# Optimization experiments

Measured on AMD Instinct MI355X. Metric: run time of the kernel, lower is better.

Reference implementation:

```python
import jax, jax.numpy as jnp
import numpy as np

B, N, S, D, H, ITERS = 32, 4096, 24, 256, 4, 3
DH = D // H
SCALE = DH ** -0.5
EPS = 1e-8
LN_EPS = 1e-5


def _ln(x, g, b):
    m = x.mean(-1, keepdims=True)
    v = ((x - m) ** 2).mean(-1, keepdims=True)
    return (x - m) * jax.lax.rsqrt(v + LN_EPS) * g + b


def setup_inputs() -> dict:
    key = jax.random.key(0)
    ks = jax.random.split(key, 20)
    xav = lambda k, fi, fo: jax.random.uniform(k, (fi, fo), jnp.float32, -1.0, 1.0) * np.sqrt(6.0 / (fi + fo))
    u = lambda k, shp, fan: jax.random.uniform(k, shp, jnp.float32, -1.0, 1.0) / np.sqrt(fan)
    return {
        "extracted_features": jax.random.normal(ks[0], (B, N, D), jnp.float32),
        "conditioning": jax.random.normal(ks[1], (B, S, D), jnp.float32),
        "pos_ln_g": jnp.ones((D,), jnp.float32),
        "pos_ln_b": jnp.zeros((D,), jnp.float32),
        "pos_w1": xav(ks[2], D, D),
        "pos_b1": jnp.zeros((D,), jnp.float32),
        "pos_w2": xav(ks[3], D, D),
        "pos_b2": jnp.zeros((D,), jnp.float32),
        "in_ln_g": jnp.ones((D,), jnp.float32),
        "in_ln_b": jnp.zeros((D,), jnp.float32),
        "slot_ln_g": jnp.ones((D,), jnp.float32),
        "slot_ln_b": jnp.zeros((D,), jnp.float32),
        "Wq": u(ks[4], (D, D), D),
        "Wk": u(ks[5], (D, D), D),
        "Wv": u(ks[6], (D, D), D),
        "gru_wi": u(ks[7], (D, 3 * D), D),  # x @ gru_wi, torch weight_ih.T
        "gru_wh": u(ks[8], (D, 3 * D), D),
        "gru_bi": u(ks[9], (3 * D,), D),
        "gru_bh": u(ks[10], (3 * D,), D),
    }


def reference(extracted_features, conditioning, pos_ln_g, pos_ln_b, pos_w1, pos_b1,
              pos_w2, pos_b2, in_ln_g, in_ln_b, slot_ln_g, slot_ln_b,
              Wq, Wk, Wv, gru_wi, gru_wh, gru_bi, gru_bh):
    b, n, _ = extracted_features.shape
    s = conditioning.shape[1]
    # positional embedding MLP: LN -> Linear -> ReLU -> Linear
    feats = _ln(extracted_features, pos_ln_g, pos_ln_b)
    feats = jax.nn.relu(feats @ pos_w1 + pos_b1) @ pos_w2 + pos_b2
    # slot attention input norm + k/v projections
    inp = _ln(feats, in_ln_g, in_ln_b)
    k = (inp @ Wk).reshape(b, n, H, DH)
    v = (inp @ Wv).reshape(b, n, H, DH)

    slots = conditioning
    attn_before = None
    for _ in range(ITERS):
        slots_prev = slots
        sn = _ln(slots, slot_ln_g, slot_ln_b)
        q = (sn @ Wq).reshape(b, s, H, DH)
        dots = jnp.einsum('bihd,bjhd->bihj', q, k) * SCALE  # [b,s,H,n]
        # softmax over flattened (slot, head) axis per input token
        attn = jax.nn.softmax(dots.reshape(b, s * H, n), axis=1).reshape(b, s, H, n)
        attn_before = attn
        attn_r = (attn + EPS)
        attn_r = attn_r / attn_r.sum(-1, keepdims=True)
        updates = jnp.einsum('bjhd,bihj->bihd', v, attn_r).reshape(b * s, D)
        # GRUCell update
        h = slots_prev.reshape(b * s, D)
        gi = updates @ gru_wi + gru_bi
        gh = h @ gru_wh + gru_bh
        ir, iz, inn = jnp.split(gi, 3, axis=-1)
        hr, hz, hn = jnp.split(gh, 3, axis=-1)
        r = jax.nn.sigmoid(ir + hr)
        z = jax.nn.sigmoid(iz + hz)
        nn_ = jnp.tanh(inn + r * hn)
        slots = ((1.0 - z) * nn_ + z * h).reshape(b, s, D)

    return slots, attn_before.mean(axis=2)
```

## Files before the change

### kernel.cpp

```cpp
#include <hip/hip_runtime.h>
#include <hip/hip_bf16.h>
#include <stdint.h>

typedef __hip_bfloat16 bf16;
typedef __attribute__((ext_vector_type(8))) short short8;
typedef __attribute__((ext_vector_type(4))) float floatx4;

#define DEV __device__ __forceinline__

DEV float bf2f(bf16 v) { return __bfloat162float(v); }
DEV bf16 f2b(float f) { return __float2bfloat16(f); }
DEV unsigned short f2bu(float f) {
  bf16 h = __float2bfloat16(f);
  union { bf16 h; unsigned short u; } c; c.h = h; return c.u;
}
DEV bool is_bf16_in(const void* probe) { return ((const unsigned short*)probe)[0] != 0; }


__global__ __launch_bounds__(256) void params_kernel(
    const void* s0, const void* s1, const void* s2, const void* s3, const void* s4,
    const void* s5, const void* s6, const void* s7, const void* s8, const void* s9,
    float* dst)
{
  int idx = blockIdx.x * 256 + threadIdx.x;
  if (idx >= 3584) return;
  bool bf = is_bf16_in(s0);
  const void* srcs[10] = {s0, s1, s2, s3, s4, s5, s6, s7, s8, s9};
  int a, off;
  if (idx < 2048)      { a = idx >> 8; off = idx & 255; }
  else if (idx < 2816) { a = 8; off = idx - 2048; }
  else                 { a = 9; off = idx - 2816; }
  float v = bf ? bf2f(((const bf16*)srcs[a])[off]) : ((const float*)srcs[a])[off];
  dst[idx] = v;
}

__global__ __launch_bounds__(256) void transpose_all_kernel(
    const void* w1, const void* w2, const void* wq, const void* wk, const void* wv,
    const void* gwi, const void* gwh,
    bf16* d1, bf16* d2, bf16* dq, bf16* dk, bf16* dv, bf16* dgi, bf16* dgh,
    const void* probe)
{
  int idx = blockIdx.x * 256 + threadIdx.x;
  if (idx >= 720896) return;
  bool bf = is_bf16_in(probe);
  const void* src; bf16* dst; int C, off;
  if (idx < 327680) {
    int wsel = idx >> 16; off = idx & 65535; C = 256;
    const void* S[5] = {w1, w2, wq, wk, wv};
    bf16* D[5] = {d1, d2, dq, dk, dv};
    src = S[wsel]; dst = D[wsel];
  } else {
    int j = idx - 327680; int wsel = j / 196608; off = j - wsel * 196608; C = 768;
    src = wsel ? gwh : gwi; dst = wsel ? dgh : dgi;
  }
  int r = off / C, c = off - r * C;
  bf16 v = bf ? ((const bf16*)src)[off] : f2b(((const float*)src)[off]);
  dst[(size_t)c * 256 + r] = v;
}

__global__ __launch_bounds__(256) void init_slots_kernel(
    const void* __restrict__ cond, float* __restrict__ sF, bf16* __restrict__ sB,
    const void* probe)
{
  int idx = blockIdx.x * 256 + threadIdx.x;
  bool bf = is_bf16_in(probe);
  float v = bf ? bf2f(((const bf16*)cond)[idx]) : ((const float*)cond)[idx];
  sF[idx] = v;
  sB[idx] = f2b(v);
}

template<bool OUT_BF16, bool RELU, bool HAS_BIAS>
DEV void gemm_body(const bf16* __restrict__ A, const bf16* __restrict__ Bt,
                   const float* __restrict__ bias, void* __restrict__ C,
                   int M, int N, int K, int bx, int by, short* As, short* Bs)
{
  const int tid = threadIdx.x;
  const int lane = tid & 63;
  const int wave = tid >> 6;
  const int wr = wave >> 1, wc = wave & 1;
  const int m16 = lane & 15, quad = lane >> 4;
  const long m0 = (long)by * 128, n0 = (long)bx * 128;

  floatx4 acc[4][4];
#pragma unroll
  for (int i = 0; i < 4; i++)
#pragma unroll
    for (int j = 0; j < 4; j++) acc[i][j] = {0.f, 0.f, 0.f, 0.f};

  const int srow = tid >> 3;
  const int scol = (tid & 7) * 8;

  for (int kb = 0; kb < K; kb += 64) {
#pragma unroll
    for (int p = 0; p < 4; p++) {
      int row = srow + p * 32;
      uint4 av = *(const uint4*)(A + (m0 + row) * (long)K + kb + scol);
      *(uint4*)(&As[row * 72 + scol]) = av;
      uint4 bv = *(const uint4*)(Bt + (n0 + row) * (long)K + kb + scol);
      *(uint4*)(&Bs[row * 72 + scol]) = bv;
    }
    __syncthreads();
#pragma unroll
    for (int ks = 0; ks < 2; ks++) {
      short8 af[4], bfr[4];
#pragma unroll
      for (int t = 0; t < 4; t++) {
        af[t]  = *(const short8*)(&As[(wr * 64 + t * 16 + m16) * 72 + ks * 32 + quad * 8]);
        bfr[t] = *(const short8*)(&Bs[(wc * 64 + t * 16 + m16) * 72 + ks * 32 + quad * 8]);
      }
#pragma unroll
      for (int mt = 0; mt < 4; mt++)
#pragma unroll
        for (int nt = 0; nt < 4; nt++)
          acc[mt][nt] = __builtin_amdgcn_mfma_f32_16x16x32_bf16(af[mt], bfr[nt], acc[mt][nt], 0, 0, 0);
    }
    __syncthreads();
  }

#pragma unroll
  for (int mt = 0; mt < 4; mt++) {
#pragma unroll
    for (int nt = 0; nt < 4; nt++) {
      long col = n0 + wc * 64 + nt * 16 + m16;
      float bb = HAS_BIAS ? bias[col] : 0.f;
#pragma unroll
      for (int r = 0; r < 4; r++) {
        long row = m0 + wr * 64 + mt * 16 + quad * 4 + r;
        float v = acc[mt][nt][r] + bb;
        if (RELU) v = fmaxf(v, 0.f);
        if (OUT_BF16) ((bf16*)C)[row * N + col] = f2b(v);
        else          ((float*)C)[row * N + col] = v;
      }
    }
  }
}

__global__ __launch_bounds__(256) void gru2_kernel(
    const bf16* __restrict__ updB, const bf16* __restrict__ sB,
    const bf16* __restrict__ gwit, const bf16* __restrict__ gwht,
    const float* __restrict__ par, float* __restrict__ gi, float* __restrict__ gh)
{
  __shared__ short As[128 * 72];
  __shared__ short Bs[128 * 72];
  if (blockIdx.z == 0)
    gemm_body<false, false, true>(updB, gwit, par + 2048, gi, 768, 768, 256,
                                  blockIdx.x, blockIdx.y, As, Bs);
  else
    gemm_body<false, false, true>(sB, gwht, par + 2816, gh, 768, 768, 256,
                                  blockIdx.x, blockIdx.y, As, Bs);
}


DEV void mm64(const short* As, const bf16* __restrict__ W,
              floatx4 acc[4][4], int wave, int m16, int quad)
{
#pragma unroll
  for (int ks = 0; ks < 8; ks++) {
    short8 af[4], bfr[4];
#pragma unroll
    for (int t = 0; t < 4; t++) {
      int row = t * 16 + m16;
      af[t] = *(const short8*)(&As[row * 256 + ((ks * 32 + quad * 8) ^ ((row & 7) << 3))]);
      bfr[t] = *(const short8*)(W + (size_t)(wave * 64 + t * 16 + m16) * 256 + ks * 32 + quad * 8);
    }
#pragma unroll
    for (int mt = 0; mt < 4; mt++)
#pragma unroll
      for (int nt = 0; nt < 4; nt++)
        acc[mt][nt] = __builtin_amdgcn_mfma_f32_16x16x32_bf16(af[mt], bfr[nt], acc[mt][nt], 0, 0, 0);
  }
}

__global__ __launch_bounds__(256, 3) void phasea_kernel(
    const void* __restrict__ x,
    const bf16* __restrict__ w1t, const bf16* __restrict__ w2t,
    const bf16* __restrict__ wkt, const bf16* __restrict__ wvt,
    const float* __restrict__ par,
    bf16* __restrict__ kbuf, bf16* __restrict__ vT, const void* probe)
{
  __shared__ short As[64 * 256];
  const int tid = threadIdx.x;
  const int lane = tid & 63;
  const int wave = tid >> 6;
  const int m16 = lane & 15, quad = lane >> 4;
  const long m0 = (long)blockIdx.x * 64;
  const bool bfin = is_bf16_in(probe);

  {
    float4 gv = *(const float4*)(par + lane * 4);
    float4 bv = *(const float4*)(par + 256 + lane * 4);
#pragma unroll
    for (int i = 0; i < 16; i++) {
      int row = wave * 16 + i;
      float v[4];
      if (bfin) {
        uint2 u = *(const uint2*)((const bf16*)x + (m0 + row) * 256 + lane * 4);
        v[0] = __uint_as_float((u.x & 0xffffu) << 16);
        v[1] = __uint_as_float(u.x & 0xffff0000u);
        v[2] = __uint_as_float((u.y & 0xffffu) << 16);
        v[3] = __uint_as_float(u.y & 0xffff0000u);
      } else {
        float4 f = *(const float4*)((const float*)x + (m0 + row) * 256 + lane * 4);
        v[0] = f.x; v[1] = f.y; v[2] = f.z; v[3] = f.w;
      }
      float s = v[0] + v[1] + v[2] + v[3];
      float sq = v[0] * v[0] + v[1] * v[1] + v[2] * v[2] + v[3] * v[3];
#pragma unroll
      for (int off = 32; off > 0; off >>= 1) { s += __shfl_xor(s, off); sq += __shfl_xor(sq, off); }
      float mn = s * (1.f / 256.f);
      float rs = rsqrtf(sq * (1.f / 256.f) - mn * mn + 1e-5f);
      union { unsigned short us[4]; uint2 u; } pk;
      pk.us[0] = f2bu((v[0] - mn) * rs * gv.x + bv.x);
      pk.us[1] = f2bu((v[1] - mn) * rs * gv.y + bv.y);
      pk.us[2] = f2bu((v[2] - mn) * rs * gv.z + bv.z);
      pk.us[3] = f2bu((v[3] - mn) * rs * gv.w + bv.w);
      *(uint2*)(&As[row * 256 + ((lane * 4) ^ ((row & 7) << 3))]) = pk.u;
    }
  }
  __syncthreads();

  floatx4 acc[4][4];

#pragma unroll
  for (int i = 0; i < 4; i++)
#pragma unroll
    for (int j = 0; j < 4; j++) acc[i][j] = {0.f, 0.f, 0.f, 0.f};
  mm64(As, w1t, acc, wave, m16, quad);
  __syncthreads();
#pragma unroll
  for (int mt = 0; mt < 4; mt++)
#pragma unroll
    for (int nt = 0; nt < 4; nt++) {
      int col = wave * 64 + nt * 16 + m16;
      float bb = par[512 + col];
#pragma unroll
      for (int r = 0; r < 4; r++) {
        int row = mt * 16 + quad * 4 + r;
        As[row * 256 + (col ^ ((row & 7) << 3))] = (short)f2bu(fmaxf(acc[mt][nt][r] + bb, 0.f));
      }
    }
  __syncthreads();

#pragma unroll
  for (int i = 0; i < 4; i++)
#pragma unroll
    for (int j = 0; j < 4; j++) acc[i][j] = {0.f, 0.f, 0.f, 0.f};
  mm64(As, w2t, acc, wave, m16, quad);
  __syncthreads();
#pragma unroll
  for (int mt = 0; mt < 4; mt++)
#pragma unroll
    for (int nt = 0; nt < 4; nt++) {
      int col = wave * 64 + nt * 16 + m16;
      float bb = par[768 + col];
#pragma unroll
      for (int r = 0; r < 4; r++) {
        int row = mt * 16 + quad * 4 + r;
        As[row * 256 + (col ^ ((row & 7) << 3))] = (short)f2bu(acc[mt][nt][r] + bb);
      }
    }
  __syncthreads();

  {
    float4 gv = *(const float4*)(par + 1024 + lane * 4);
    float4 bv = *(const float4*)(par + 1280 + lane * 4);
#pragma unroll
    for (int i = 0; i < 16; i++) {
      int row = wave * 16 + i;
      int ci = (lane * 4) ^ ((row & 7) << 3);
      uint2 u = *(const uint2*)(&As[row * 256 + ci]);
      float v[4];
      v[0] = __uint_as_float((u.x & 0xffffu) << 16);
      v[1] = __uint_as_float(u.x & 0xffff0000u);
      v[2] = __uint_as_float((u.y & 0xffffu) << 16);
      v[3] = __uint_as_float(u.y & 0xffff0000u);
      float s = v[0] + v[1] + v[2] + v[3];
      float sq = v[0] * v[0] + v[1] * v[1] + v[2] * v[2] + v[3] * v[3];
#pragma unroll
      for (int off = 32; off > 0; off >>= 1) { s += __shfl_xor(s, off); sq += __shfl_xor(sq, off); }
      float mn = s * (1.f / 256.f);
      float rs = rsqrtf(sq * (1.f / 256.f) - mn * mn + 1e-5f);
      union { unsigned short us[4]; uint2 u; } pk;
      pk.us[0] = f2bu((v[0] - mn) * rs * gv.x + bv.x);
      pk.us[1] = f2bu((v[1] - mn) * rs * gv.y + bv.y);
      pk.us[2] = f2bu((v[2] - mn) * rs * gv.z + bv.z);
      pk.us[3] = f2bu((v[3] - mn) * rs * gv.w + bv.w);
      *(uint2*)(&As[row * 256 + ci]) = pk.u;
    }
  }
  __syncthreads();

#pragma unroll
  for (int i = 0; i < 4; i++)
#pragma unroll
    for (int j = 0; j < 4; j++) acc[i][j] = {0.f, 0.f, 0.f, 0.f};
  mm64(As, wkt, acc, wave, m16, quad);
#pragma unroll
  for (int mt = 0; mt < 4; mt++)
#pragma unroll
    for (int nt = 0; nt < 4; nt++) {
      int col = wave * 64 + nt * 16 + m16;
#pragma unroll
      for (int r = 0; r < 4; r++) {
        long row = m0 + mt * 16 + quad * 4 + r;
        kbuf[row * 256 + col] = f2b(acc[mt][nt][r]);
      }
    }

#pragma unroll
  for (int i = 0; i < 4; i++)
#pragma unroll
    for (int j = 0; j < 4; j++) acc[i][j] = {0.f, 0.f, 0.f, 0.f};
  mm64(As, wvt, acc, wave, m16, quad);
  __syncthreads();
#pragma unroll
  for (int mt = 0; mt < 4; mt++)
#pragma unroll
    for (int nt = 0; nt < 4; nt++) {
      int d = wave * 64 + nt * 16 + m16;
      int t = mt * 16 + quad * 4;
      union { unsigned short us[4]; uint2 u; } pk;
#pragma unroll
      for (int r = 0; r < 4; r++) pk.us[r] = f2bu(acc[mt][nt][r]);
      *(uint2*)(&As[d * 64 + (t ^ ((d & 15) << 2))]) = pk.u;
    }
  __syncthreads();

  {
    int sub = lane >> 4;
    int mcol = lane & 15;
#pragma unroll
    for (int j = 0; j < 16; j++) {
      int d = wave * 64 + j * 4 + sub;
      int t = mcol * 4;
      uint2 u = *(const uint2*)(&As[d * 64 + (t ^ ((d & 15) << 2))]);
      *(uint2*)(vT + (size_t)d * 131072 + m0 + t) = u;
    }
  }
}

__global__ __launch_bounds__(256) void lnq_kernel(
    const float* __restrict__ sF, const bf16* __restrict__ wqt,
    const float* __restrict__ par, bf16* __restrict__ qp)
{
  __shared__ short As[32 * 264];
  const int tid = threadIdx.x;
  const int lane = tid & 63;
  const int wave = tid >> 6;
  const int m16 = lane & 15, quad = lane >> 4;
  const int b = blockIdx.x;

  for (int i = tid; i < 8 * 264; i += 256) As[24 * 264 + i] = 0;

  float4 gv = *(const float4*)(par + 1536 + lane * 4);
  float4 bv = *(const float4*)(par + 1792 + lane * 4);
#pragma unroll
  for (int i = 0; i < 6; i++) {
    int row = wave * 6 + i;
    float4 f = *(const float4*)(sF + ((size_t)(b * 24 + row)) * 256 + lane * 4);
    float v[4] = {f.x, f.y, f.z, f.w};
    float s = v[0] + v[1] + v[2] + v[3];
    float sq = v[0] * v[0] + v[1] * v[1] + v[2] * v[2] + v[3] * v[3];
#pragma unroll
    for (int off = 32; off > 0; off >>= 1) { s += __shfl_xor(s, off); sq += __shfl_xor(sq, off); }
    float mn = s * (1.f / 256.f);
    float rs = rsqrtf(sq * (1.f / 256.f) - mn * mn + 1e-5f);
    union { unsigned short us[4]; uint2 u; } pk;
    pk.us[0] = f2bu((v[0] - mn) * rs * gv.x + bv.x);
    pk.us[1] = f2bu((v[1] - mn) * rs * gv.y + bv.y);
    pk.us[2] = f2bu((v[2] - mn) * rs * gv.z + bv.z);
    pk.us[3] = f2bu((v[3] - mn) * rs * gv.w + bv.w);
    *(uint2*)(&As[row * 264 + lane * 4]) = pk.u;
  }
  __syncthreads();

  floatx4 acc[2][4];
#pragma unroll
  for (int i = 0; i < 2; i++)
#pragma unroll
    for (int j = 0; j < 4; j++) acc[i][j] = {0.f, 0.f, 0.f, 0.f};
#pragma unroll
  for (int ks = 0; ks < 8; ks++) {
    short8 af[2], bfr[4];
#pragma unroll
    for (int mt = 0; mt < 2; mt++)
      af[mt] = *(const short8*)(&As[(mt * 16 + m16) * 264 + ks * 32 + quad * 8]);
#pragma unroll
    for (int nt = 0; nt < 4; nt++)
      bfr[nt] = *(const short8*)(wqt + (size_t)(wave * 64 + nt * 16 + m16) * 256 + ks * 32 + quad * 8);
#pragma unroll
    for (int mt = 0; mt < 2; mt++)
#pragma unroll
      for (int nt = 0; nt < 4; nt++)
        acc[mt][nt] = __builtin_amdgcn_mfma_f32_16x16x32_bf16(af[mt], bfr[nt], acc[mt][nt], 0, 0, 0);
  }

  bf16* qpb = qp + (size_t)(b * 4 + wave) * 2048;
#pragma unroll
  for (int mt = 0; mt < 2; mt++)
#pragma unroll
    for (int nt = 0; nt < 4; nt++)
#pragma unroll
      for (int r = 0; r < 4; r++) {
        int m = mt * 16 + quad * 4 + r;
        qpb[m * 64 + nt * 16 + m16] = f2b(acc[mt][nt][r] * 0.125f);
      }
}

template<bool LAST>
__global__ __launch_bounds__(256) void attn_iter_kernel(
    const bf16* __restrict__ qp, const bf16* __restrict__ kbuf,
    const bf16* __restrict__ vT, float* __restrict__ pupd,
    void* __restrict__ out, const void* __restrict__ probe)
{
  const int js = blockIdx.x;
  const int b  = blockIdx.y;
  const int h  = threadIdx.x >> 6;
  const int lane = threadIdx.x & 63;
  const int m16 = lane & 15, quad = lane >> 4;

  __shared__ unsigned short att[4 * 24 * 136];
  __shared__ float red1[4 * 132];
  __shared__ float red2[4 * 132];

  short8 qf[2][2];
  const bf16* qpb = qp + (size_t)(b * 4 + h) * 2048;
#pragma unroll
  for (int mt = 0; mt < 2; mt++)
#pragma unroll
    for (int ks = 0; ks < 2; ks++)
      qf[mt][ks] = *(const short8*)(qpb + (mt * 16 + m16) * 64 + ks * 32 + quad * 8);

  const bool mt1_valid = (quad < 2);
  int arow1 = 16 + m16; if (arow1 > 23) arow1 = 23;

  floatx4 uacc[2][4];
#pragma unroll
  for (int i = 0; i < 2; i++)
#pragma unroll
    for (int j = 0; j < 4; j++) uacc[i][j] = {0.f, 0.f, 0.f, 0.f};
  float wsum[2][4] = {{0.f, 0.f, 0.f, 0.f}, {0.f, 0.f, 0.f, 0.f}};

  for (int hh = 0; hh < 2; hh++) {
    const int j0 = js * 256 + hh * 128;

    floatx4 dacc[2][8];
#pragma unroll
    for (int i = 0; i < 2; i++)
#pragma unroll
      for (int j = 0; j < 8; j++) dacc[i][j] = {0.f, 0.f, 0.f, 0.f};

    const bf16* kb = kbuf + ((size_t)b * 4096 + j0) * 256 + h * 64;
#pragma unroll
    for (int ks = 0; ks < 2; ks++)
#pragma unroll
      for (int nt = 0; nt < 8; nt++) {
        short8 bfr = *(const short8*)(kb + (size_t)(nt * 16 + m16) * 256 + ks * 32 + quad * 8);
        dacc[0][nt] = __builtin_amdgcn_mfma_f32_16x16x32_bf16(qf[0][ks], bfr, dacc[0][nt], 0, 0, 0);
        dacc[1][nt] = __builtin_amdgcn_mfma_f32_16x16x32_bf16(qf[1][ks], bfr, dacc[1][nt], 0, 0, 0);
      }

    float cmax[8];
#pragma unroll
    for (int nt = 0; nt < 8; nt++) {
      float m = fmaxf(fmaxf(dacc[0][nt][0], dacc[0][nt][1]), fmaxf(dacc[0][nt][2], dacc[0][nt][3]));
      if (mt1_valid)
        m = fmaxf(m, fmaxf(fmaxf(dacc[1][nt][0], dacc[1][nt][1]), fmaxf(dacc[1][nt][2], dacc[1][nt][3])));
      m = fmaxf(m, __shfl_xor(m, 16));
      m = fmaxf(m, __shfl_xor(m, 32));
      cmax[nt] = m;
    }
    if (quad == 0) {
#pragma unroll
      for (int nt = 0; nt < 8; nt++) red1[h * 132 + nt * 16 + m16] = cmax[nt];
    }
    __syncthreads();

    float csum[8];
#pragma unroll
    for (int nt = 0; nt < 8; nt++) {
      int c = nt * 16 + m16;
      float g = fmaxf(fmaxf(red1[c], red1[132 + c]), fmaxf(red1[264 + c], red1[396 + c]));
      float s = 0.f;
#pragma unroll
      for (int r = 0; r < 4; r++) {
        float e = __expf(dacc[0][nt][r] - g);
        dacc[0][nt][r] = e; s += e;
      }
#pragma unroll
      for (int r = 0; r < 4; r++) {
        float e = mt1_valid ? __expf(dacc[1][nt][r] - g) : 0.f;
        dacc[1][nt][r] = e; s += e;
      }
      s += __shfl_xor(s, 16);
      s += __shfl_xor(s, 32);
      csum[nt] = s;
    }
    if (quad == 0) {
#pragma unroll
      for (int nt = 0; nt < 8; nt++) red2[h * 132 + nt * 16 + m16] = csum[nt];
    }
    __syncthreads();

#pragma unroll
    for (int nt = 0; nt < 8; nt++) {
      int c = nt * 16 + m16;
      float inv = 1.f / (red2[c] + red2[132 + c] + red2[264 + c] + red2[396 + c]);
#pragma unroll
      for (int r = 0; r < 4; r++) {
        float a = dacc[0][nt][r] * inv + 1e-8f;
        att[h * 3264 + (quad * 4 + r) * 136 + c] = f2bu(a);
        wsum[0][r] += a;
      }
      if (mt1_valid) {
#pragma unroll
        for (int r = 0; r < 4; r++) {
          float a = dacc[1][nt][r] * inv + 1e-8f;
          att[h * 3264 + (16 + quad * 4 + r) * 136 + c] = f2bu(a);
          wsum[1][r] += a;
        }
      }
    }
    __syncthreads();

    const bf16* vb0 = vT + (size_t)b * 4096 + j0;
#pragma unroll
    for (int ks = 0; ks < 4; ks++) {
      short8 a0 = *(const short8*)(&att[h * 3264 + m16 * 136 + ks * 32 + quad * 8]);
      short8 a1 = *(const short8*)(&att[h * 3264 + arow1 * 136 + ks * 32 + quad * 8]);
#pragma unroll
      for (int nt = 0; nt < 4; nt++) {
        short8 bfr = *(const short8*)(vb0 + (size_t)(h * 64 + nt * 16 + m16) * 131072 + ks * 32 + quad * 8);
        uacc[0][nt] = __builtin_amdgcn_mfma_f32_16x16x32_bf16(a0, bfr, uacc[0][nt], 0, 0, 0);
        uacc[1][nt] = __builtin_amdgcn_mfma_f32_16x16x32_bf16(a1, bfr, uacc[1][nt], 0, 0, 0);
      }
    }

    if (LAST) {
      const bool bfo = is_bf16_in(probe);
      int c = threadIdx.x & 127;
      int half = threadIdx.x >> 7;
#pragma unroll
      for (int i0 = 0; i0 < 12; i0++) {
        int i = half * 12 + i0;
        float s = bf2f(__ushort_as_bfloat16(att[i * 136 + c]))
                + bf2f(__ushort_as_bfloat16(att[3264 + i * 136 + c]))
                + bf2f(__ushort_as_bfloat16(att[6528 + i * 136 + c]))
                + bf2f(__ushort_as_bfloat16(att[9792 + i * 136 + c]));
        size_t oidx = ((size_t)(b * 24 + i)) * 4096 + j0 + c;
        if (bfo) ((bf16*)out)[196608 + oidx] = f2b(0.25f * s);
        else     ((float*)out)[196608 + oidx] = 0.25f * s;
      }
    }
    __syncthreads();
  }

  float* dst = pupd + ((size_t)((b * 4 + h) * 16 + js)) * 1920;
#pragma unroll
  for (int mt = 0; mt < 2; mt++)
#pragma unroll
    for (int r = 0; r < 4; r++) {
      float w = wsum[mt][r];
      w += __shfl_xor(w, 1); w += __shfl_xor(w, 2);
      w += __shfl_xor(w, 4); w += __shfl_xor(w, 8);
      wsum[mt][r] = w;
    }
  if (m16 == 0) {
#pragma unroll
    for (int mt = 0; mt < 2; mt++)
#pragma unroll
      for (int r = 0; r < 4; r++) {
        int row = mt * 16 + quad * 4 + r;
        if (row < 24) dst[row * 80 + 64] = wsum[mt][r];
      }
  }
#pragma unroll
  for (int mt = 0; mt < 2; mt++)
#pragma unroll
    for (int nt = 0; nt < 4; nt++)
#pragma unroll
      for (int r = 0; r < 4; r++) {
        int row = mt * 16 + quad * 4 + r;
        if (row < 24) dst[row * 80 + nt * 16 + m16] = uacc[mt][nt][r];
      }
}

__global__ __launch_bounds__(256) void upd_final_kernel(
    const float* __restrict__ pupd, bf16* __restrict__ updB)
{
  int bh = blockIdx.x; int b = bh >> 2, h = bh & 3;
  int idx = blockIdx.y * 256 + threadIdx.x;
  int i = idx >> 6, d = idx & 63;
  const float* base = pupd + (size_t)bh * 16 * 1920 + i * 80;
  float v = 0.f, w = 0.f;
#pragma unroll
  for (int p = 0; p < 16; p++) {
    v += base[p * 1920 + d];
    w += base[p * 1920 + 64];
  }
  updB[((size_t)(b * 24 + i)) * 256 + h * 64 + d] = f2b(v / w);
}

template<bool LAST>
__global__ __launch_bounds__(256) void gru_gate_kernel(
    const float* __restrict__ gi, const float* __restrict__ gh,
    float* __restrict__ sF, bf16* __restrict__ sB,
    void* __restrict__ out, const void* __restrict__ probe)
{
  int row = blockIdx.x, d = threadIdx.x;
  size_t o = (size_t)row * 768;
  float ir = gi[o + d], iz = gi[o + 256 + d], inn = gi[o + 512 + d];
  float hr = gh[o + d], hz = gh[o + 256 + d], hn = gh[o + 512 + d];
  float hv = sF[(size_t)row * 256 + d];
  float r = 1.f / (1.f + __expf(-(ir + hr)));
  float z = 1.f / (1.f + __expf(-(iz + hz)));
  float nn = tanhf(inn + r * hn);
  float sv = (1.f - z) * nn + z * hv;
  sF[(size_t)row * 256 + d] = sv;
  sB[(size_t)row * 256 + d] = f2b(sv);
  if (LAST) {
    if (is_bf16_in(probe)) ((bf16*)out)[(size_t)row * 256 + d] = f2b(sv);
    else                   ((float*)out)[(size_t)row * 256 + d] = sv;
  }
}

static constexpr size_t SZ_BIG   = (size_t)32 * 4096 * 256 * 2;
static constexpr size_t OFF_BUF1 = 0;
static constexpr size_t OFF_BUF2 = OFF_BUF1 + SZ_BIG;
static constexpr size_t OFF_K    = OFF_BUF2 + SZ_BIG;
static constexpr size_t OFF_V    = OFF_K + SZ_BIG;
static constexpr size_t OFF_Q    = OFF_V + SZ_BIG;
static constexpr size_t OFF_QP   = OFF_Q + (size_t)768 * 256 * 4;
static constexpr size_t OFF_SNB  = OFF_QP + (size_t)32 * 4 * 32 * 64 * 2;
static constexpr size_t OFF_SF   = OFF_SNB + (size_t)768 * 256 * 2;
static constexpr size_t OFF_SB   = OFF_SF + (size_t)768 * 256 * 4;
static constexpr size_t OFF_UPD  = OFF_SB + (size_t)768 * 256 * 2;
static constexpr size_t OFF_GI   = OFF_UPD + (size_t)768 * 256 * 2;
static constexpr size_t OFF_GH   = OFF_GI + (size_t)768 * 768 * 4;
static constexpr size_t OFF_PUPD = OFF_GH + (size_t)768 * 768 * 4;
static constexpr size_t OFF_W1T  = OFF_PUPD + (size_t)128 * 32 * 1920 * 4;
static constexpr size_t OFF_W2T  = OFF_W1T + (size_t)256 * 256 * 2;
static constexpr size_t OFF_WQT  = OFF_W2T + (size_t)256 * 256 * 2;
static constexpr size_t OFF_WKT  = OFF_WQT + (size_t)256 * 256 * 2;
static constexpr size_t OFF_WVT  = OFF_WKT + (size_t)256 * 256 * 2;
static constexpr size_t OFF_GWIT = OFF_WVT + (size_t)256 * 256 * 2;
static constexpr size_t OFF_GWHT = OFF_GWIT + (size_t)256 * 768 * 2;
static constexpr size_t OFF_PAR  = OFF_GWHT + (size_t)256 * 768 * 2;
static constexpr size_t OFF_FLAG = OFF_PAR + (size_t)3584 * 4;
static constexpr size_t WS_NEED  = OFF_FLAG + 256;

extern "C" void kernel_launch(void* const* d_in, const int* in_sizes, int n_in,
                              void* d_out, int out_size, void* d_ws, size_t ws_size,
                              hipStream_t stream) {
  (void)in_sizes; (void)n_in; (void)out_size;
  if (ws_size < WS_NEED) return;

  const void* x         = d_in[0];
  const void* cond      = d_in[1];
  const void* pos_ln_g  = d_in[2];
  const void* pos_ln_b  = d_in[3];
  const void* pos_w1    = d_in[4];
  const void* pos_b1    = d_in[5];
  const void* pos_w2    = d_in[6];
  const void* pos_b2    = d_in[7];
  const void* in_ln_g   = d_in[8];
  const void* in_ln_b   = d_in[9];
  const void* slot_ln_g = d_in[10];
  const void* slot_ln_b = d_in[11];
  const void* Wq        = d_in[12];
  const void* Wk        = d_in[13];
  const void* Wv        = d_in[14];
  const void* gru_wi    = d_in[15];
  const void* gru_wh    = d_in[16];
  const void* gru_bi    = d_in[17];
  const void* gru_bh    = d_in[18];

  char* ws = (char*)d_ws;
  bf16*  kbuf  = (bf16*)(ws + OFF_K);
  bf16*  vT    = (bf16*)(ws + OFF_V);
  bf16*  qp    = (bf16*)(ws + OFF_QP);
  float* sF    = (float*)(ws + OFF_SF);
  bf16*  sB    = (bf16*)(ws + OFF_SB);
  bf16*  updB  = (bf16*)(ws + OFF_UPD);
  float* gi    = (float*)(ws + OFF_GI);
  float* gh    = (float*)(ws + OFF_GH);
  float* pupd  = (float*)(ws + OFF_PUPD);
  bf16*  w1t   = (bf16*)(ws + OFF_W1T);
  bf16*  w2t   = (bf16*)(ws + OFF_W2T);
  bf16*  wqt   = (bf16*)(ws + OFF_WQT);
  bf16*  wkt   = (bf16*)(ws + OFF_WKT);
  bf16*  wvt   = (bf16*)(ws + OFF_WVT);
  bf16*  gwit  = (bf16*)(ws + OFF_GWIT);
  bf16*  gwht  = (bf16*)(ws + OFF_GWHT);
  float* par   = (float*)(ws + OFF_PAR);

  const void* probe = pos_ln_g;

  params_kernel<<<14, 256, 0, stream>>>(pos_ln_g, pos_ln_b, pos_b1, pos_b2,
                                        in_ln_g, in_ln_b, slot_ln_g, slot_ln_b,
                                        gru_bi, gru_bh, par);
  transpose_all_kernel<<<2816, 256, 0, stream>>>(pos_w1, pos_w2, Wq, Wk, Wv, gru_wi, gru_wh,
                                                 w1t, w2t, wqt, wkt, wvt, gwit, gwht, probe);
  init_slots_kernel<<<768, 256, 0, stream>>>(cond, sF, sB, probe);

  phasea_kernel<<<2048, 256, 0, stream>>>(x, w1t, w2t, wkt, wvt, par, kbuf, vT, probe);

  for (int it = 0; it < 3; it++) {
    lnq_kernel<<<32, 256, 0, stream>>>(sF, wqt, par, qp);
    if (it == 2)
      attn_iter_kernel<true><<<dim3(16, 32), 256, 0, stream>>>(qp, kbuf, vT, pupd, d_out, probe);
    else
      attn_iter_kernel<false><<<dim3(16, 32), 256, 0, stream>>>(qp, kbuf, vT, pupd, d_out, probe);
    upd_final_kernel<<<dim3(128, 6), 256, 0, stream>>>(pupd, updB);
    gru2_kernel<<<dim3(6, 6, 2), 256, 0, stream>>>(updB, sB, gwit, gwht, par, gi, gh);
    if (it == 2)
      gru_gate_kernel<true><<<768, 256, 0, stream>>>(gi, gh, sF, sB, d_out, probe);
    else
      gru_gate_kernel<false><<<768, 256, 0, stream>>>(gi, gh, sF, sB, d_out, probe);
  }
}
```

Measured before the change: 674.1 us.

## Stage weights through double-buffered LDS in 128-token phase-A blocks with coalesced stores

Phase A (LN, two-layer MLP, LN, K/V projections) now processes 128 tokens per 512-thread block using a 2x4 wave grid. Weight tiles are staged into swizzled, double-buffered shared memory in 64-wide K slices, with the next slice prefetched while the current one is computed. Previously every wave read its weight fragments directly from global memory. K and V outputs are staged in LDS and written with 16-byte coalesced stores instead of scattered 2-byte K stores. The cost is 128 KB of LDS per block and more barriers, which limits occupancy to at most one or two blocks per CU.

```diff
diff --git a/kernel.cpp b/kernel.cpp
--- a/kernel.cpp
+++ b/kernel.cpp
@@ -151,17 +151,37 @@
 }
 
 
-DEV void mm64(const short* As, const bf16* __restrict__ W,
-              floatx4 acc[4][4], int wave, int m16, int quad)
-{
-#pragma unroll
-  for (int ks = 0; ks < 8; ks++) {
+DEV void pa_loadB(uint4 r[4], const bf16* __restrict__ W, int sk, int tid)
+{
+#pragma unroll
+  for (int p = 0; p < 4; p++) {
+    int idx = p * 512 + tid;
+    int n = idx >> 3, k8 = idx & 7;
+    r[p] = *(const uint4*)(W + (size_t)n * 256 + sk * 64 + ((k8 ^ (n & 7)) << 3));
+  }
+}
+DEV void pa_writeB(short* BsBuf, const uint4 r[4], int tid)
+{
+#pragma unroll
+  for (int p = 0; p < 4; p++) {
+    int idx = p * 512 + tid;
+    int n = idx >> 3, k8 = idx & 7;
+    *(uint4*)(&BsBuf[n * 64 + (k8 << 3)]) = r[p];
+  }
+}
+
+DEV void pa_slice(const short* At, const short* BsBuf, int sk,
+                  int wr, int wc, int m16, int quad, floatx4 acc[4][4])
+{
+#pragma unroll
+  for (int ks = 0; ks < 2; ks++) {
     short8 af[4], bfr[4];
 #pragma unroll
     for (int t = 0; t < 4; t++) {
-      int row = t * 16 + m16;
-      af[t] = *(const short8*)(&As[row * 256 + ((ks * 32 + quad * 8) ^ ((row & 7) << 3))]);
-      bfr[t] = *(const short8*)(W + (size_t)(wave * 64 + t * 16 + m16) * 256 + ks * 32 + quad * 8);
+      int row = wr * 64 + t * 16 + m16;
+      af[t] = *(const short8*)(&At[row * 256 + ((sk * 64 + ks * 32 + quad * 8) ^ ((row & 7) << 3))]);
+      int n = wc * 64 + t * 16 + m16;
+      bfr[t] = *(const short8*)(&BsBuf[n * 64 + ((ks * 32 + quad * 8) ^ ((n & 7) << 3))]);
     }
 #pragma unroll
     for (int mt = 0; mt < 4; mt++)
@@ -171,19 +191,67 @@
   }
 }
 
-__global__ __launch_bounds__(256, 3) void phasea_kernel(
+DEV void pa_gemm(const short* At, short* Bs, const bf16* __restrict__ W,
+                 int tid, int wr, int wc, int m16, int quad, floatx4 acc[4][4])
+{
+  uint4 r[4];
+  pa_loadB(r, W, 0, tid);
+  pa_writeB(Bs, r, tid);
+  __syncthreads();
+#pragma unroll
+  for (int s = 0; s < 4; s++) {
+    if (s < 3) pa_loadB(r, W, s + 1, tid);
+    pa_slice(At, Bs + (s & 1) * 16384, s, wr, wc, m16, quad, acc);
+    if (s < 3) pa_writeB(Bs + ((s + 1) & 1) * 16384, r, tid);
+    __syncthreads();
+  }
+}
+
+DEV void pa_ln_inplace(short* At, const float* __restrict__ par, int goff,
+                       int wave, int lane)
+{
+  float4 gv = *(const float4*)(par + goff + lane * 4);
+  float4 bv = *(const float4*)(par + goff + 256 + lane * 4);
+#pragma unroll
+  for (int i = 0; i < 16; i++) {
+    int row = wave * 16 + i;
+    int ci = (lane * 4) ^ ((row & 7) << 3);
+    uint2 u = *(const uint2*)(&At[row * 256 + ci]);
+    float v[4];
+    v[0] = __uint_as_float((u.x & 0xffffu) << 16);
+    v[1] = __uint_as_float(u.x & 0xffff0000u);
+    v[2] = __uint_as_float((u.y & 0xffffu) << 16);
+    v[3] = __uint_as_float(u.y & 0xffff0000u);
+    float s = v[0] + v[1] + v[2] + v[3];
+    float sq = v[0] * v[0] + v[1] * v[1] + v[2] * v[2] + v[3] * v[3];
+#pragma unroll
+    for (int off = 32; off > 0; off >>= 1) { s += __shfl_xor(s, off); sq += __shfl_xor(sq, off); }
+    float mn = s * (1.f / 256.f);
+    float rs = rsqrtf(sq * (1.f / 256.f) - mn * mn + 1e-5f);
+    union { unsigned short us[4]; uint2 u; } pk;
+    pk.us[0] = f2bu((v[0] - mn) * rs * gv.x + bv.x);
+    pk.us[1] = f2bu((v[1] - mn) * rs * gv.y + bv.y);
+    pk.us[2] = f2bu((v[2] - mn) * rs * gv.z + bv.z);
+    pk.us[3] = f2bu((v[3] - mn) * rs * gv.w + bv.w);
+    *(uint2*)(&At[row * 256 + ci]) = pk.u;
+  }
+}
+
+__global__ __launch_bounds__(512, 2) void phasea_kernel(
     const void* __restrict__ x,
     const bf16* __restrict__ w1t, const bf16* __restrict__ w2t,
     const bf16* __restrict__ wkt, const bf16* __restrict__ wvt,
     const float* __restrict__ par,
     bf16* __restrict__ kbuf, bf16* __restrict__ vT, const void* probe)
 {
-  __shared__ short As[64 * 256];
+  __shared__ short At[128 * 256];
+  __shared__ short Bs[2 * 16384];
   const int tid = threadIdx.x;
   const int lane = tid & 63;
   const int wave = tid >> 6;
+  const int wr = wave >> 2, wc = wave & 3;
   const int m16 = lane & 15, quad = lane >> 4;
-  const long m0 = (long)blockIdx.x * 64;
+  const long m0 = (long)blockIdx.x * 128;
   const bool bfin = is_bf16_in(probe);
 
   {
@@ -214,128 +282,88 @@
       pk.us[1] = f2bu((v[1] - mn) * rs * gv.y + bv.y);
       pk.us[2] = f2bu((v[2] - mn) * rs * gv.z + bv.z);
       pk.us[3] = f2bu((v[3] - mn) * rs * gv.w + bv.w);
-      *(uint2*)(&As[row * 256 + ((lane * 4) ^ ((row & 7) << 3))]) = pk.u;
-    }
-  }
+      *(uint2*)(&At[row * 256 + ((lane * 4) ^ ((row & 7) << 3))]) = pk.u;
+    }
+  }
+
+  floatx4 acc[4][4];
+
+#pragma unroll
+  for (int i = 0; i < 4; i++)
+#pragma unroll
+    for (int j = 0; j < 4; j++) acc[i][j] = {0.f, 0.f, 0.f, 0.f};
+  pa_gemm(At, Bs, w1t, tid, wr, wc, m16, quad, acc);
+#pragma unroll
+  for (int mt = 0; mt < 4; mt++)
+#pragma unroll
+    for (int nt = 0; nt < 4; nt++) {
+      int col = wc * 64 + nt * 16 + m16;
+      float bb = par[512 + col];
+#pragma unroll
+      for (int r = 0; r < 4; r++) {
+        int row = wr * 64 + mt * 16 + quad * 4 + r;
+        At[row * 256 + (col ^ ((row & 7) << 3))] = (short)f2bu(fmaxf(acc[mt][nt][r] + bb, 0.f));
+      }
+    }
   __syncthreads();
 
-  floatx4 acc[4][4];
-
 #pragma unroll
   for (int i = 0; i < 4; i++)
 #pragma unroll
     for (int j = 0; j < 4; j++) acc[i][j] = {0.f, 0.f, 0.f, 0.f};
-  mm64(As, w1t, acc, wave, m16, quad);
+  pa_gemm(At, Bs, w2t, tid, wr, wc, m16, quad, acc);
+#pragma unroll
+  for (int mt = 0; mt < 4; mt++)
+#pragma unroll
+    for (int nt = 0; nt < 4; nt++) {
+      int col = wc * 64 + nt * 16 + m16;
+      float bb = par[768 + col];
+#pragma unroll
+      for (int r = 0; r < 4; r++) {
+        int row = wr * 64 + mt * 16 + quad * 4 + r;
+        At[row * 256 + (col ^ ((row & 7) << 3))] = (short)f2bu(acc[mt][nt][r] + bb);
+      }
+    }
   __syncthreads();
+
+  pa_ln_inplace(At, par, 1024, wave, lane);
+  __syncthreads();
+
+  floatx4 acc4[4][4];
+#pragma unroll
+  for (int i = 0; i < 4; i++)
+#pragma unroll
+    for (int j = 0; j < 4; j++) { acc[i][j] = {0.f, 0.f, 0.f, 0.f}; acc4[i][j] = {0.f, 0.f, 0.f, 0.f}; }
+  pa_gemm(At, Bs, wkt, tid, wr, wc, m16, quad, acc);
+  pa_gemm(At, Bs, wvt, tid, wr, wc, m16, quad, acc4);
+
 #pragma unroll
   for (int mt = 0; mt < 4; mt++)
 #pragma unroll
     for (int nt = 0; nt < 4; nt++) {
-      int col = wave * 64 + nt * 16 + m16;
-      float bb = par[512 + col];
-#pragma unroll
-      for (int r = 0; r < 4; r++) {
-        int row = mt * 16 + quad * 4 + r;
-        As[row * 256 + (col ^ ((row & 7) << 3))] = (short)f2bu(fmaxf(acc[mt][nt][r] + bb, 0.f));
-      }
+      int tokb = wr * 64 + mt * 16 + quad * 4;
+      int d = wc * 64 + nt * 16 + m16;
+#pragma unroll
+      for (int r = 0; r < 4; r++) {
+        int tok = tokb + r;
+        At[tok * 256 + (d ^ ((tok & 7) << 3))] = (short)f2bu(acc[mt][nt][r]);
+      }
+      union { unsigned short us[4]; uint2 u; } pk;
+#pragma unroll
+      for (int r = 0; r < 4; r++) pk.us[r] = f2bu(acc4[mt][nt][r]);
+      *(uint2*)(&Bs[d * 128 + (tokb ^ ((d & 15) << 3))]) = pk.u;
     }
   __syncthreads();
 
 #pragma unroll
-  for (int i = 0; i < 4; i++)
-#pragma unroll
-    for (int j = 0; j < 4; j++) acc[i][j] = {0.f, 0.f, 0.f, 0.f};
-  mm64(As, w2t, acc, wave, m16, quad);
-  __syncthreads();
-#pragma unroll
-  for (int mt = 0; mt < 4; mt++)
-#pragma unroll
-    for (int nt = 0; nt < 4; nt++) {
-      int col = wave * 64 + nt * 16 + m16;
-      float bb = par[768 + col];
-#pragma unroll
-      for (int r = 0; r < 4; r++) {
-        int row = mt * 16 + quad * 4 + r;
-        As[row * 256 + (col ^ ((row & 7) << 3))] = (short)f2bu(acc[mt][nt][r] + bb);
-      }
-    }
-  __syncthreads();
-
-  {
-    float4 gv = *(const float4*)(par + 1024 + lane * 4);
-    float4 bv = *(const float4*)(par + 1280 + lane * 4);
-#pragma unroll
-    for (int i = 0; i < 16; i++) {
-      int row = wave * 16 + i;
-      int ci = (lane * 4) ^ ((row & 7) << 3);
-      uint2 u = *(const uint2*)(&As[row * 256 + ci]);
-      float v[4];
-      v[0] = __uint_as_float((u.x & 0xffffu) << 16);
-      v[1] = __uint_as_float(u.x & 0xffff0000u);
-      v[2] = __uint_as_float((u.y & 0xffffu) << 16);
-      v[3] = __uint_as_float(u.y & 0xffff0000u);
-      float s = v[0] + v[1] + v[2] + v[3];
-      float sq = v[0] * v[0] + v[1] * v[1] + v[2] * v[2] + v[3] * v[3];
-#pragma unroll
-      for (int off = 32; off > 0; off >>= 1) { s += __shfl_xor(s, off); sq += __shfl_xor(sq, off); }
-      float mn = s * (1.f / 256.f);
-      float rs = rsqrtf(sq * (1.f / 256.f) - mn * mn + 1e-5f);
-      union { unsigned short us[4]; uint2 u; } pk;
-      pk.us[0] = f2bu((v[0] - mn) * rs * gv.x + bv.x);
-      pk.us[1] = f2bu((v[1] - mn) * rs * gv.y + bv.y);
-      pk.us[2] = f2bu((v[2] - mn) * rs * gv.z + bv.z);
-      pk.us[3] = f2bu((v[3] - mn) * rs * gv.w + bv.w);
-      *(uint2*)(&As[row * 256 + ci]) = pk.u;
-    }
-  }
-  __syncthreads();
-
-#pragma unroll
-  for (int i = 0; i < 4; i++)
-#pragma unroll
-    for (int j = 0; j < 4; j++) acc[i][j] = {0.f, 0.f, 0.f, 0.f};
-  mm64(As, wkt, acc, wave, m16, quad);
-#pragma unroll
-  for (int mt = 0; mt < 4; mt++)
-#pragma unroll
-    for (int nt = 0; nt < 4; nt++) {
-      int col = wave * 64 + nt * 16 + m16;
-#pragma unroll
-      for (int r = 0; r < 4; r++) {
-        long row = m0 + mt * 16 + quad * 4 + r;
-        kbuf[row * 256 + col] = f2b(acc[mt][nt][r]);
-      }
-    }
-
-#pragma unroll
-  for (int i = 0; i < 4; i++)
-#pragma unroll
-    for (int j = 0; j < 4; j++) acc[i][j] = {0.f, 0.f, 0.f, 0.f};
-  mm64(As, wvt, acc, wave, m16, quad);
-  __syncthreads();
-#pragma unroll
-  for (int mt = 0; mt < 4; mt++)
-#pragma unroll
-    for (int nt = 0; nt < 4; nt++) {
-      int d = wave * 64 + nt * 16 + m16;
-      int t = mt * 16 + quad * 4;
-      union { unsigned short us[4]; uint2 u; } pk;
-#pragma unroll
-      for (int r = 0; r < 4; r++) pk.us[r] = f2bu(acc[mt][nt][r]);
-      *(uint2*)(&As[d * 64 + (t ^ ((d & 15) << 2))]) = pk.u;
-    }
-  __syncthreads();
-
-  {
-    int sub = lane >> 4;
-    int mcol = lane & 15;
-#pragma unroll
-    for (int j = 0; j < 16; j++) {
-      int d = wave * 64 + j * 4 + sub;
-      int t = mcol * 4;
-      uint2 u = *(const uint2*)(&As[d * 64 + (t ^ ((d & 15) << 2))]);
-      *(uint2*)(vT + (size_t)d * 131072 + m0 + t) = u;
-    }
+  for (int rr = 0; rr < 8; rr++) {
+    int idx = rr * 512 + tid;
+    int tok = idx >> 5, dg = (idx & 31) * 8;
+    uint4 kv = *(const uint4*)(&At[tok * 256 + (dg ^ ((tok & 7) << 3))]);
+    *(uint4*)(kbuf + (m0 + tok) * 256 + dg) = kv;
+    int d = idx >> 4, tg = (idx & 15) * 8;
+    uint4 vv = *(const uint4*)(&Bs[d * 128 + (tg ^ ((d & 15) << 3))]);
+    *(uint4*)(vT + (size_t)d * 131072 + m0 + tg) = vv;
   }
 }
 
@@ -703,7 +731,7 @@
                                                  w1t, w2t, wqt, wkt, wvt, gwit, gwht, probe);
   init_slots_kernel<<<768, 256, 0, stream>>>(cond, sF, sB, probe);
 
-  phasea_kernel<<<2048, 256, 0, stream>>>(x, w1t, w2t, wkt, wvt, par, kbuf, vT, probe);
+  phasea_kernel<<<1024, 512, 0, stream>>>(x, w1t, w2t, wkt, wvt, par, kbuf, vT, probe);
 
   for (int it = 0; it < 3; it++) {
     lnq_kernel<<<32, 256, 0, stream>>>(sF, wqt, par, qp);
```

Measured after the change: 586.0 us. 13.1% less time.
